# Kernel optimization log

Hardware: AMD Instinct MI355X
Metric: run time of the kernel (lower is better)

The kernel has to match this reference:

```python
import jax, jax.numpy as jnp
import numpy as np

GRID_SIZE = 16
KH = KW = 3


def setup_inputs() -> dict:
    key = jax.random.key(0)
    k1, k2, k3, k4 = jax.random.split(key, 4)
    B, H, W, C, F = 8, 32, 32, 64, 64
    x = jax.random.normal(k1, (B, H, W, C), dtype=jnp.float32)
    control_points = jax.random.normal(k2, (F, C, KH, KW, GRID_SIZE), dtype=jnp.float32) * 0.1
    w1 = jax.random.normal(k3, (F, C, KH, KW), dtype=jnp.float32) * 0.1
    w2 = jax.random.normal(k4, (F, C, KH, KW), dtype=jnp.float32) * 0.1
    return {"x": x, "control_points": control_points, "w1": w1, "w2": w2}


def _extract_patches_same(x, kh, kw):
    # x: (B,H,W,C), stride 1, TF 'SAME' padding -> (B,H,W,kh,kw,C)
    B, H, W, C = x.shape
    ph, pw = kh - 1, kw - 1
    xp = jnp.pad(x, ((0, 0), (ph // 2, ph - ph // 2), (pw // 2, pw - pw // 2), (0, 0)))
    taps = [xp[:, i:i + H, j:j + W, :] for i in range(kh) for j in range(kw)]
    return jnp.stack(taps, axis=3).reshape(B, H, W, kh, kw, C)


def reference(x, control_points, w1, w2):
    F, C, kh, kw, G = control_points.shape
    grid = jnp.linspace(-1.0, 1.0, G)
    patches = _extract_patches_same(x, kh, kw)  # (B,H,W,kh,kw,C)
    # spline: searchsorted + clip + linear interp on the fixed uniform grid
    xc = jnp.clip(patches, -1.0, 1.0)
    idx = jnp.clip(jnp.searchsorted(grid, xc, side='left') - 1, 0, G - 2)
    frac = (xc - grid[idx]) / (grid[idx + 1] - grid[idx])  # (B,H,W,kh,kw,C)
    # two-nonzero linear basis over control points -> (B,H,W,kh,kw,C,G)
    basis = (jax.nn.one_hot(idx, G, dtype=x.dtype) * (1.0 - frac)[..., None]
             + jax.nn.one_hot(idx + 1, G, dtype=x.dtype) * frac[..., None])
    # fuse w1 into control points, contract taps+channels+grid in one einsum
    wcp = w1[..., None] * control_points  # (F,C,kh,kw,G)
    out = jnp.einsum('bpqijcg,fcijg->bpqf', basis, wcp)
    out = out + jnp.einsum('bpqijc,fcij->bpqf', jax.nn.silu(patches), w2)
    return out  # (B,H,W,F)
```

## Files before the change

### kernel.cpp

```cpp
#include <hip/hip_runtime.h>


typedef _Float16 v8h __attribute__((ext_vector_type(8)));
typedef float    v4f __attribute__((ext_vector_type(4)));

#define NSLOT   655360
#define PARTOFF 1310720
#define NPART   524288

__global__ __launch_bounds__(256) void prep_wsw(const float* __restrict__ cp,
                                                const float* __restrict__ w1,
                                                const float* __restrict__ w2,
                                                _Float16* __restrict__ wsw) {
    int tid  = blockIdx.x * 256 + threadIdx.x;
    int j    = tid & 7;
    int lane = (tid >> 3) & 63;
    int rest = tid >> 9;
    int nt   = rest & 3;
    int ks   = rest >> 2;
    int k    = ks * 32 + ((lane >> 4) << 3) + j;
    int f    = (nt << 4) + (lane & 15);
    int chunk = k / 640;
    int kl    = k - chunk * 640;
    float val = 0.f;
    if (kl < 576) {
        int c = (chunk << 2) + kl / 144;
        int r = kl % 144;
        val = w1[f * 576 + c * 9 + (r >> 4)] * cp[f * 9216 + c * 144 + r];
    } else {
        int i2 = kl - 576;
        int ij = i2 & 15;
        if (ij < 9) {
            int c = (chunk << 2) + (i2 >> 4);
            val = w2[f * 576 + c * 9 + ij];
        }
    }
    wsw[tid] = (_Float16)val;
}

__global__ __launch_bounds__(256, 3) void kan_mfma(const float* __restrict__ x,
                                                   const _Float16* __restrict__ wsw,
                                                   float* __restrict__ part) {
    __shared__ __align__(16) char smem[41472];
    _Float16* sb  = (_Float16*)smem;
    float*    red = (float*)smem;

    int blk   = blockIdx.x;
    int kh    = blk >> 8;
    int rowid = blk & 255;
    int b = rowid >> 5, p = rowid & 31;
    int t = threadIdx.x, wv = t >> 6, lane = t & 63;
    int m = lane & 15, kq = lane >> 4;

    const int chs[4] = {0, 6, 11, 16};
    int ch0 = chs[kh], ch1 = chs[kh + 1];

    v4f z4 = (v4f){0.f, 0.f, 0.f, 0.f};
    for (int i4 = t; i4 < 2592; i4 += 256) ((v4f*)sb)[i4] = z4;

    const float* xb = x + (size_t)b * 65536;
    int  off0[5], sbF[5], sil[5];
    bool okv[5];
#pragma unroll
    for (int it = 0; it < 5; ++it) {
        int e  = t + it * 256;
        int ec = e < 1152 ? e : 0;
        int px = ec / 36;
        int r  = ec - px * 36;
        int cl = r / 9;
        int ij = r - cl * 9;
        int di = ij / 3;
        int dj = ij - di * 3;
        int row = p + di - 1;
        int col = px + dj - 1;
        okv[it]  = ((unsigned)row < 32u) && ((unsigned)col < 32u) && (e < 1152);
        off0[it] = okv[it] ? ((row * 32 + col) * 64 + cl) : 0;
        sbF[it]  = px * 648 + cl * 144 + ij * 16;
        sil[it]  = px * 648 + 576 + cl * 16 + ij;
    }

    v4f acc[2][4];
#pragma unroll
    for (int i = 0; i < 2; ++i)
#pragma unroll
        for (int n = 0; n < 4; ++n) acc[i][n] = z4;

    float vbuf[5];
#pragma unroll
    for (int it = 0; it < 5; ++it)
        vbuf[it] = okv[it] ? xb[off0[it] + ch0 * 4] : 0.f;

    __syncthreads();

    for (int gch = ch0; gch < ch1; ++gch) {
#pragma unroll
        for (int it = 0; it < 5; ++it) {
            if (t + it * 256 < 1152) {
                float v  = vbuf[it];
                float xc = fminf(fmaxf(v, -1.f), 1.f);
                float tt = (xc + 1.f) * 7.5f;
                int idx  = (int)tt;
                if (idx > 14) idx = 14;
                float fr = tt - (float)idx;
                float sv = v * __builtin_amdgcn_rcpf(1.f + __expf(-v));
                _Float16 hg = (_Float16)(1.f - fr);
                _Float16 hf = (_Float16)fr;
                _Float16 hz = (_Float16)0.f;
                v8h row0, row1;
#pragma unroll
                for (int g = 0; g < 8; ++g)
                    row0[g] = (g == idx) ? hg : ((g == idx + 1) ? hf : hz);
#pragma unroll
                for (int g = 8; g < 16; ++g)
                    row1[g - 8] = (g == idx) ? hg : ((g == idx + 1) ? hf : hz);
                *(v8h*)(sb + sbF[it])     = row0;
                *(v8h*)(sb + sbF[it] + 8) = row1;
                sb[sil[it]] = (_Float16)sv;
            }
        }
        if (gch + 1 < ch1) {
#pragma unroll
            for (int it = 0; it < 5; ++it)
                vbuf[it] = okv[it] ? xb[off0[it] + (gch + 1) * 4] : 0.f;
        }
        __syncthreads();
        const _Float16* ap0 = sb + m * 648 + (wv * 5) * 32 + kq * 8;
        const v8h* bp = (const v8h*)wsw + ((size_t)gch * 20 + wv * 5) * 256 + lane;
#pragma unroll
        for (int s = 0; s < 5; ++s) {
            v8h a0 = *(const v8h*)(ap0 + s * 32);
            v8h a1 = *(const v8h*)(ap0 + s * 32 + 16 * 648);
            v8h b0 = bp[s * 256];
            v8h b1 = bp[s * 256 + 64];
            v8h b2 = bp[s * 256 + 128];
            v8h b3 = bp[s * 256 + 192];
            acc[0][0] = __builtin_amdgcn_mfma_f32_16x16x32_f16(a0, b0, acc[0][0], 0, 0, 0);
            acc[0][1] = __builtin_amdgcn_mfma_f32_16x16x32_f16(a0, b1, acc[0][1], 0, 0, 0);
            acc[0][2] = __builtin_amdgcn_mfma_f32_16x16x32_f16(a0, b2, acc[0][2], 0, 0, 0);
            acc[0][3] = __builtin_amdgcn_mfma_f32_16x16x32_f16(a0, b3, acc[0][3], 0, 0, 0);
            acc[1][0] = __builtin_amdgcn_mfma_f32_16x16x32_f16(a1, b0, acc[1][0], 0, 0, 0);
            acc[1][1] = __builtin_amdgcn_mfma_f32_16x16x32_f16(a1, b1, acc[1][1], 0, 0, 0);
            acc[1][2] = __builtin_amdgcn_mfma_f32_16x16x32_f16(a1, b2, acc[1][2], 0, 0, 0);
            acc[1][3] = __builtin_amdgcn_mfma_f32_16x16x32_f16(a1, b3, acc[1][3], 0, 0, 0);
        }
        __syncthreads();
    }

#pragma unroll
    for (int mt = 0; mt < 2; ++mt)
#pragma unroll
        for (int nt = 0; nt < 4; ++nt)
#pragma unroll
            for (int r = 0; r < 4; ++r)
                red[wv * 2080 + (mt * 16 + kq * 4 + r) * 65 + nt * 16 + m] = acc[mt][nt][r];
    __syncthreads();
    int f = t & 63, pxg = t >> 6;
    float* op = part + (size_t)kh * NPART + rowid * 2048 + f;
#pragma unroll
    for (int i = 0; i < 8; ++i) {
        int px = pxg * 8 + i;
        float s = red[px * 65 + f] + red[2080 + px * 65 + f]
                + red[4160 + px * 65 + f] + red[6240 + px * 65 + f];
        op[px * 64] = s;
    }
}

__global__ __launch_bounds__(256) void combine(const float* __restrict__ part,
                                               float* __restrict__ out) {
    int i = blockIdx.x * 256 + threadIdx.x;
    v4f a = ((const v4f*)part)[i];
    v4f b = ((const v4f*)(part + NPART))[i];
    v4f c = ((const v4f*)(part + 2 * NPART))[i];
    ((v4f*)out)[i] = a + b + c;
}

extern "C" void kernel_launch(void* const* d_in, const int* in_sizes, int n_in,
                              void* d_out, int out_size, void* d_ws, size_t ws_size,
                              hipStream_t stream) {
    const float* x  = (const float*)d_in[0];
    const float* cp = (const float*)d_in[1];
    const float* w1 = (const float*)d_in[2];
    const float* w2 = (const float*)d_in[3];
    _Float16* wsw = (_Float16*)d_ws;
    float*    prt = (float*)((char*)d_ws + PARTOFF);

    prep_wsw<<<NSLOT / 256, 256, 0, stream>>>(cp, w1, w2, wsw);
    kan_mfma<<<768, 256, 0, stream>>>(x, wsw, prt);
    combine<<<512, 256, 0, stream>>>(prt, (float*)d_out);
}
```

Baseline: 92.88 us.

## Retile KAN MFMA to 64-pixel blocks, six-way K split, drop LDS reduction

Each block now covers two output rows (64 pixels), and each wave owns 16 pixels over the full per-block K range, so the LDS cross-wave reduction and its extra barrier go away. Channels are split six ways instead of three, with a per-block rotated start channel to spread weight reads across blocks. The weight layout is repacked into 2-channel chunks, and the combine kernel now sums six partials. In exchange, each wave reuses every loaded weight fragment over half as many pixels, the partial buffers and combine traffic double, and the larger workspace must fit.

New measurement: 103.3 us. 11.2% more time.

```diff
diff --git a/kernel.cpp b/kernel.cpp
--- a/kernel.cpp
+++ b/kernel.cpp
@@ -20,20 +20,20 @@
     int ks   = rest >> 2;
     int k    = ks * 32 + ((lane >> 4) << 3) + j;
     int f    = (nt << 4) + (lane & 15);
-    int chunk = k / 640;
-    int kl    = k - chunk * 640;
+    int chunk = k / 320;
+    int kl    = k - chunk * 320;
     float val = 0.f;
-    if (kl < 576) {
-        int c = (chunk << 2) + kl / 144;
-        int r = kl % 144;
+    if (kl < 288) {
+        int cl = kl / 144;
+        int r  = kl - cl * 144;
+        int c  = chunk * 2 + cl;
         val = w1[f * 576 + c * 9 + (r >> 4)] * cp[f * 9216 + c * 144 + r];
-    } else {
-        int i2 = kl - 576;
-        int ij = i2 & 15;
-        if (ij < 9) {
-            int c = (chunk << 2) + (i2 >> 4);
-            val = w2[f * 576 + c * 9 + ij];
-        }
+    } else if (kl < 306) {
+        int i2 = kl - 288;
+        int cl = i2 / 9;
+        int ij = i2 - cl * 9;
+        int c  = chunk * 2 + cl;
+        val = w2[f * 576 + c * 9 + ij];
     }
     wsw[tid] = (_Float16)val;
 }
@@ -41,58 +41,61 @@
 __global__ __launch_bounds__(256, 3) void kan_mfma(const float* __restrict__ x,
                                                    const _Float16* __restrict__ wsw,
                                                    float* __restrict__ part) {
-    __shared__ __align__(16) char smem[41472];
-    _Float16* sb  = (_Float16*)smem;
-    float*    red = (float*)smem;
+    __shared__ __align__(16) _Float16 sb[64 * 328];
 
-    int blk   = blockIdx.x;
-    int kh    = blk >> 8;
-    int rowid = blk & 255;
-    int b = rowid >> 5, p = rowid & 31;
+    int blk = blockIdx.x;
+    int kh  = blk >> 7;
+    int mb  = blk & 127;
+    int b     = mb >> 4;
+    int prow0 = (mb & 15) << 1;
     int t = threadIdx.x, wv = t >> 6, lane = t & 63;
     int m = lane & 15, kq = lane >> 4;
 
-    const int chs[4] = {0, 6, 11, 16};
+    const int chs[7] = {0, 6, 12, 17, 22, 27, 32};
     int ch0 = chs[kh], ch1 = chs[kh + 1];
+    int nch = ch1 - ch0;
+    int rot = mb % nch;
 
     v4f z4 = (v4f){0.f, 0.f, 0.f, 0.f};
-    for (int i4 = t; i4 < 2592; i4 += 256) ((v4f*)sb)[i4] = z4;
+    for (int i4 = t; i4 < 2624; i4 += 256) ((v4f*)sb)[i4] = z4;
 
-    const float* xb = x + (size_t)b * 65536;
     int  off0[5], sbF[5], sil[5];
     bool okv[5];
 #pragma unroll
     for (int it = 0; it < 5; ++it) {
         int e  = t + it * 256;
         int ec = e < 1152 ? e : 0;
-        int px = ec / 36;
-        int r  = ec - px * 36;
+        int px = ec / 18;
+        int r  = ec - px * 18;
         int cl = r / 9;
         int ij = r - cl * 9;
         int di = ij / 3;
         int dj = ij - di * 3;
+        int p   = prow0 + (px >> 5);
+        int q   = px & 31;
         int row = p + di - 1;
-        int col = px + dj - 1;
+        int col = q + dj - 1;
         okv[it]  = ((unsigned)row < 32u) && ((unsigned)col < 32u) && (e < 1152);
-        off0[it] = okv[it] ? ((row * 32 + col) * 64 + cl) : 0;
-        sbF[it]  = px * 648 + cl * 144 + ij * 16;
-        sil[it]  = px * 648 + 576 + cl * 16 + ij;
+        off0[it] = okv[it] ? (((b * 32 + row) * 32 + col) * 64 + cl) : 0;
+        sbF[it]  = px * 328 + cl * 144 + ij * 16;
+        sil[it]  = px * 328 + 288 + cl * 9 + ij;
     }
 
-    v4f acc[2][4];
+    v4f acc[4];
 #pragma unroll
-    for (int i = 0; i < 2; ++i)
-#pragma unroll
-        for (int n = 0; n < 4; ++n) acc[i][n] = z4;
+    for (int n = 0; n < 4; ++n) acc[n] = z4;
 
+    int gch0 = ch0 + rot;
+    if (gch0 >= ch1) gch0 -= nch;
     float vbuf[5];
 #pragma unroll
     for (int it = 0; it < 5; ++it)
-        vbuf[it] = okv[it] ? xb[off0[it] + ch0 * 4] : 0.f;
+        vbuf[it] = okv[it] ? x[off0[it] + gch0 * 2] : 0.f;
 
     __syncthreads();
 
-    for (int gch = ch0; gch < ch1; ++gch) {
+    int gch = gch0;
+    for (int ci = 0; ci < nch; ++ci) {
 #pragma unroll
         for (int it = 0; it < 5; ++it) {
             if (t + it * 256 < 1152) {
@@ -118,60 +121,47 @@
                 sb[sil[it]] = (_Float16)sv;
             }
         }
-        if (gch + 1 < ch1) {
+        int gnx = gch + 1;
+        if (gnx >= ch1) gnx = ch0;
+        if (ci + 1 < nch) {
 #pragma unroll
             for (int it = 0; it < 5; ++it)
-                vbuf[it] = okv[it] ? xb[off0[it] + (gch + 1) * 4] : 0.f;
+                vbuf[it] = okv[it] ? x[off0[it] + gnx * 2] : 0.f;
         }
         __syncthreads();
-        const _Float16* ap0 = sb + m * 648 + (wv * 5) * 32 + kq * 8;
-        const v8h* bp = (const v8h*)wsw + ((size_t)gch * 20 + wv * 5) * 256 + lane;
+        const _Float16* ap0 = sb + (wv * 16 + m) * 328 + kq * 8;
+        const v8h* bp = (const v8h*)wsw + (size_t)(gch * 10) * 256 + lane;
 #pragma unroll
-        for (int s = 0; s < 5; ++s) {
-            v8h a0 = *(const v8h*)(ap0 + s * 32);
-            v8h a1 = *(const v8h*)(ap0 + s * 32 + 16 * 648);
-            v8h b0 = bp[s * 256];
-            v8h b1 = bp[s * 256 + 64];
-            v8h b2 = bp[s * 256 + 128];
-            v8h b3 = bp[s * 256 + 192];
-            acc[0][0] = __builtin_amdgcn_mfma_f32_16x16x32_f16(a0, b0, acc[0][0], 0, 0, 0);
-            acc[0][1] = __builtin_amdgcn_mfma_f32_16x16x32_f16(a0, b1, acc[0][1], 0, 0, 0);
-            acc[0][2] = __builtin_amdgcn_mfma_f32_16x16x32_f16(a0, b2, acc[0][2], 0, 0, 0);
-            acc[0][3] = __builtin_amdgcn_mfma_f32_16x16x32_f16(a0, b3, acc[0][3], 0, 0, 0);
-            acc[1][0] = __builtin_amdgcn_mfma_f32_16x16x32_f16(a1, b0, acc[1][0], 0, 0, 0);
-            acc[1][1] = __builtin_amdgcn_mfma_f32_16x16x32_f16(a1, b1, acc[1][1], 0, 0, 0);
-            acc[1][2] = __builtin_amdgcn_mfma_f32_16x16x32_f16(a1, b2, acc[1][2], 0, 0, 0);
-            acc[1][3] = __builtin_amdgcn_mfma_f32_16x16x32_f16(a1, b3, acc[1][3], 0, 0, 0);
+        for (int s = 0; s < 10; ++s) {
+            v8h a = *(const v8h*)(ap0 + s * 32);
+            acc[0] = __builtin_amdgcn_mfma_f32_16x16x32_f16(a, bp[s * 256],       acc[0], 0, 0, 0);
+            acc[1] = __builtin_amdgcn_mfma_f32_16x16x32_f16(a, bp[s * 256 + 64],  acc[1], 0, 0, 0);
+            acc[2] = __builtin_amdgcn_mfma_f32_16x16x32_f16(a, bp[s * 256 + 128], acc[2], 0, 0, 0);
+            acc[3] = __builtin_amdgcn_mfma_f32_16x16x32_f16(a, bp[s * 256 + 192], acc[3], 0, 0, 0);
         }
         __syncthreads();
+        gch = gnx;
     }
 
+    float* op = part + (size_t)kh * NPART + (size_t)(mb * 64) * 64;
 #pragma unroll
-    for (int mt = 0; mt < 2; ++mt)
+    for (int nt = 0; nt < 4; ++nt)
 #pragma unroll
-        for (int nt = 0; nt < 4; ++nt)
-#pragma unroll
-            for (int r = 0; r < 4; ++r)
-                red[wv * 2080 + (mt * 16 + kq * 4 + r) * 65 + nt * 16 + m] = acc[mt][nt][r];
-    __syncthreads();
-    int f = t & 63, pxg = t >> 6;
-    float* op = part + (size_t)kh * NPART + rowid * 2048 + f;
-#pragma unroll
-    for (int i = 0; i < 8; ++i) {
-        int px = pxg * 8 + i;
-        float s = red[px * 65 + f] + red[2080 + px * 65 + f]
-                + red[4160 + px * 65 + f] + red[6240 + px * 65 + f];
-        op[px * 64] = s;
-    }
+        for (int r = 0; r < 4; ++r) {
+            int px = wv * 16 + kq * 4 + r;
+            int f  = nt * 16 + m;
+            op[px * 64 + f] = acc[nt][r];
+        }
 }
 
 __global__ __launch_bounds__(256) void combine(const float* __restrict__ part,
                                                float* __restrict__ out) {
     int i = blockIdx.x * 256 + threadIdx.x;
-    v4f a = ((const v4f*)part)[i];
-    v4f b = ((const v4f*)(part + NPART))[i];
-    v4f c = ((const v4f*)(part + 2 * NPART))[i];
-    ((v4f*)out)[i] = a + b + c;
+    v4f s = ((const v4f*)part)[i];
+#pragma unroll
+    for (int kh = 1; kh < 6; ++kh)
+        s += ((const v4f*)(part + (size_t)kh * NPART))[i];
+    ((v4f*)out)[i] = s;
 }
 
 extern "C" void kernel_launch(void* const* d_in, const int* in_sizes, int n_in,
```
